# Kernel optimization log

Measured on AMD Instinct MI355X. Metric: run time of the kernel, lower is better.

The kernel has to match this reference:

```python
import jax, jax.numpy as jnp
import numpy as np

# static config (levels=4, CDA=False branch -> self_attn_4, scale=4, f=False)
SHAPES = [(80, 80), (40, 40), (20, 20), (10, 10)]
D = 256; NH = 8; NL = 4; NP = 4; DFF = 1024; DH = D // NH
L = sum(h * w for h, w in SHAPES)  # 8500
B = 1


def layer_norm(x, g, b, eps=1e-5):
    m = jnp.mean(x, axis=-1, keepdims=True)
    v = jnp.mean((x - m) ** 2, axis=-1, keepdims=True)
    return (x - m) * jax.lax.rsqrt(v + eps) * g + b


def ms_deform_attn_core(value, loc, attn):
    # value: [B, L, NH, DH]; loc: [B, Lq, NH, NL, NP, 2] in [0,1]; attn: [B, Lq, NH, NL, NP]
    Bq, Lq = loc.shape[0], loc.shape[1]
    out = jnp.zeros((Bq, NH, Lq, DH), value.dtype)
    start = 0
    for lvl, (Hl, Wl) in enumerate(SHAPES):
        v = value[:, start:start + Hl * Wl]          # [B, HW, NH, DH]
        start += Hl * Wl
        v = v.transpose(0, 2, 1, 3)                  # [B, NH, HW, DH]
        ll = loc[:, :, :, lvl]                       # [B, Lq, NH, NP, 2]
        # grid_sample semantics: align_corners=False, padding_mode='zeros'
        x = ll[..., 0] * Wl - 0.5
        y = ll[..., 1] * Hl - 0.5
        x0 = jnp.floor(x); y0 = jnp.floor(y)
        acc = jnp.zeros((Bq, NH, Lq, NP, DH), value.dtype)
        for dy in (0, 1):
            for dx in (0, 1):
                xi = x0 + dx; yi = y0 + dy
                w = (1.0 - jnp.abs(x - xi)) * (1.0 - jnp.abs(y - yi))  # [B,Lq,NH,NP]
                valid = (xi >= 0) & (xi < Wl) & (yi >= 0) & (yi < Hl)
                xi_c = jnp.clip(xi, 0, Wl - 1).astype(jnp.int32)
                yi_c = jnp.clip(yi, 0, Hl - 1).astype(jnp.int32)
                lin = (yi_c * Wl + xi_c).transpose(0, 2, 1, 3).reshape(Bq, NH, Lq * NP)
                g = jnp.take_along_axis(v, lin[..., None], axis=2).reshape(Bq, NH, Lq, NP, DH)
                wv = (w * valid.astype(w.dtype)).transpose(0, 2, 1, 3)[..., None]
                acc = acc + g * wv
        aw = attn[:, :, :, lvl].transpose(0, 2, 1, 3)[..., None]  # [B,NH,Lq,NP,1]
        out = out + jnp.sum(acc * aw, axis=3)
    return out.transpose(0, 2, 1, 3).reshape(Bq, Lq, NH * DH)


def setup_inputs():
    key = jax.random.key(0)
    ks = jax.random.split(key, 24)
    s = 0.02
    d = {}
    d['src'] = jax.random.normal(ks[0], (B, L, D), jnp.float32)
    d['pos'] = jax.random.normal(ks[1], (B, L, D), jnp.float32)
    d['reference_points'] = jax.random.uniform(ks[2], (B, L, NL, 2), jnp.float32)
    d['spatial_shapes'] = jnp.array(SHAPES, jnp.int32)
    d['level_start_index'] = jnp.array(np.cumsum([0] + [h * w for h, w in SHAPES[:-1]]), jnp.int32)
    d['scale'] = 4
    # MSDeformAttn params
    d['Wo'] = jax.random.normal(ks[3], (D, NH * NL * NP * 2), jnp.float32) * s
    d['bo'] = jax.random.normal(ks[4], (NH * NL * NP * 2,), jnp.float32) * s
    d['Wa'] = jax.random.normal(ks[5], (D, NH * NL * NP), jnp.float32) * s
    d['ba'] = jax.random.normal(ks[6], (NH * NL * NP,), jnp.float32) * s
    d['Wv'] = jax.random.normal(ks[7], (D, D), jnp.float32) * s
    d['bv'] = jnp.zeros((D,), jnp.float32)
    d['Wout'] = jax.random.normal(ks[8], (D, D), jnp.float32) * s
    d['bout'] = jnp.zeros((D,), jnp.float32)
    # FFN + LayerNorms
    d['W1'] = jax.random.normal(ks[9], (D, DFF), jnp.float32) * s
    d['b1'] = jnp.zeros((DFF,), jnp.float32)
    d['W2'] = jax.random.normal(ks[10], (DFF, D), jnp.float32) * s
    d['b2'] = jnp.zeros((D,), jnp.float32)
    d['g1'] = jnp.ones((D,), jnp.float32); d['be1'] = jnp.zeros((D,), jnp.float32)
    d['g2'] = jnp.ones((D,), jnp.float32); d['be2'] = jnp.zeros((D,), jnp.float32)
    return d


def reference(src, pos, reference_points, spatial_shapes, level_start_index, scale,
              Wo, bo, Wa, ba, Wv, bv, Wout, bout, W1, b1, W2, b2, g1, be1, g2, be2):
    Bq, Lq, _ = src.shape
    q = src + pos  # with_pos_embed
    # sampling offsets & attention weights (softmax over levels*points)
    off = (q @ Wo + bo).reshape(Bq, Lq, NH, NL, NP, 2)
    attn = jax.nn.softmax((q @ Wa + ba).reshape(Bq, Lq, NH, NL * NP), axis=-1)
    attn = attn.reshape(Bq, Lq, NH, NL, NP)
    value = (src @ Wv + bv).reshape(Bq, L, NH, DH)
    # offset normalizer is (W, H) per level
    normalizer = jnp.stack([spatial_shapes[:, 1], spatial_shapes[:, 0]], -1).astype(src.dtype)
    loc = reference_points[:, :, None, :, None, :] + off / normalizer[None, None, None, :, None, :]
    src2 = ms_deform_attn_core(value, loc, attn) @ Wout + bout
    # residual + norm1 (dropout = eval identity)
    x = layer_norm(src + src2, g1, be1)
    # FFN
    ffn = jax.nn.relu(x @ W1 + b1) @ W2 + b2
    x = layer_norm(x + ffn, g2, be2)
    return x
```

## Files before the change

kernel.cpp:

```cpp
#include <hip/hip_runtime.h>
#include <hip/hip_bf16.h>
#include <string.h>

#define D 256
#define NH 8
#define DH 32
#define NL 4
#define NP 4
#define DFF 1024
#define LTOT 8500

typedef __bf16 bf16x8 __attribute__((ext_vector_type(8)));
typedef float floatx4 __attribute__((ext_vector_type(4)));

__device__ inline unsigned bpack(float a, float b) {
    __hip_bfloat16 ha = __float2bfloat16(a), hb = __float2bfloat16(b);
    unsigned short ua, ub;
    memcpy(&ua, &ha, 2); memcpy(&ub, &hb, 2);
    return (unsigned)ua | ((unsigned)ub << 16);
}

__global__ void prep(const float* __restrict__ src, const float* __restrict__ pos,
                     unsigned* __restrict__ qb, unsigned* __restrict__ srcb, int n4) {
    int i = blockIdx.x * blockDim.x + threadIdx.x;
    if (i >= n4) return;
    float4 s = *(const float4*)(src + i * 4);
    float4 p = *(const float4*)(pos + i * 4);
    uint2 sb, qb2;
    sb.x = bpack(s.x, s.y); sb.y = bpack(s.z, s.w);
    qb2.x = bpack(s.x + p.x, s.y + p.y); qb2.y = bpack(s.z + p.z, s.w + p.w);
    *(uint2*)(srcb + i * 2) = sb;
    *(uint2*)(qb + i * 2) = qb2;
}

__global__ void transpose_all(const float* W0, const float* W1_, const float* W2_,
                              const float* W3, const float* W4, const float* W5,
                              __hip_bfloat16* T0, __hip_bfloat16* T1, __hip_bfloat16* T2,
                              __hip_bfloat16* T3, __hip_bfloat16* T4, __hip_bfloat16* T5) {
    const int cum[7] = {0, 64, 96, 160, 224, 480, 736};
    int id = blockIdx.x;
    int mi = 0;
    while (id >= cum[mi + 1]) mi++;
    int lid = id - cum[mi];
    const float* W; __hip_bfloat16* T; int K, N;
    switch (mi) {
        case 0: W = W0; T = T0; K = 256;  N = 256;  break;
        case 1: W = W1_; T = T1; K = 256; N = 128;  break;
        case 2: W = W2_; T = T2; K = 256; N = 256;  break;
        case 3: W = W3; T = T3; K = 256;  N = 256;  break;
        case 4: W = W4; T = T4; K = 256;  N = 1024; break;
        default: W = W5; T = T5; K = 1024; N = 256; break;
    }
    int ntx = N >> 5;
    int n0 = (lid % ntx) * 32, k0 = (lid / ntx) * 32;
    __shared__ float t[32][33];
    int tx = threadIdx.x & 31, ty = threadIdx.x >> 5;
#pragma unroll
    for (int i = 0; i < 32; i += 8)
        t[ty + i][tx] = W[(size_t)(k0 + ty + i) * N + n0 + tx];
    __syncthreads();
#pragma unroll
    for (int i = 0; i < 32; i += 8)
        T[(size_t)(n0 + ty + i) * K + k0 + tx] = __float2bfloat16(t[tx][ty + i]);
}

template<int BM, int BN>
__global__ __launch_bounds__(256) void gemm_mfma(
    const __hip_bfloat16* __restrict__ A, const __hip_bfloat16* __restrict__ BT,
    const float* __restrict__ bias, float* __restrict__ Cf, __hip_bfloat16* __restrict__ Cb,
    int M, int N, int K, int relu) {
    constexpr int BK = 32;
    constexpr int LDA = BK + 8;
    __shared__ __hip_bfloat16 sA[BM * LDA];
    __shared__ __hip_bfloat16 sB[BN * LDA];

    int tid = threadIdx.x;
    int wave = tid >> 6, lane = tid & 63;
    int m0 = blockIdx.y * BM;
    int n0 = blockIdx.x * BN;
    constexpr int WM = BM / 2, WN = BN / 2;
    int wm = (wave >> 1) * WM;
    int wn = (wave & 1) * WN;
    constexpr int TM = WM / 16, TN = WN / 16;

    floatx4 acc[TM][TN];
#pragma unroll
    for (int i = 0; i < TM; i++)
#pragma unroll
        for (int j = 0; j < TN; j++)
#pragma unroll
            for (int e = 0; e < 4; e++) acc[i][j][e] = 0.f;

    constexpr int RA = BM / 64, RB = BN / 64;
    int rowT = tid >> 2;
    int c16 = tid & 3;
    int lrow = lane & 15;
    int lk = (lane >> 4) * 8;

    for (int k0 = 0; k0 < K; k0 += BK) {
#pragma unroll
        for (int r = 0; r < RA; r++) {
            int row = r * 64 + rowT;
            int grow = m0 + row; if (grow >= M) grow = M - 1;
            bf16x8 v = *(const bf16x8*)(A + (size_t)grow * K + k0 + c16 * 8);
            *(bf16x8*)(&sA[row * LDA + c16 * 8]) = v;
        }
#pragma unroll
        for (int r = 0; r < RB; r++) {
            int row = r * 64 + rowT;
            bf16x8 v = *(const bf16x8*)(BT + (size_t)(n0 + row) * K + k0 + c16 * 8);
            *(bf16x8*)(&sB[row * LDA + c16 * 8]) = v;
        }
        __syncthreads();

        bf16x8 af[TM], bfr[TN];
#pragma unroll
        for (int tm = 0; tm < TM; tm++)
            af[tm] = *(const bf16x8*)(&sA[(wm + tm * 16 + lrow) * LDA + lk]);
#pragma unroll
        for (int tn = 0; tn < TN; tn++)
            bfr[tn] = *(const bf16x8*)(&sB[(wn + tn * 16 + lrow) * LDA + lk]);
#pragma unroll
        for (int tm = 0; tm < TM; tm++)
#pragma unroll
            for (int tn = 0; tn < TN; tn++)
                acc[tm][tn] = __builtin_amdgcn_mfma_f32_16x16x32_bf16(af[tm], bfr[tn], acc[tm][tn], 0, 0, 0);
        __syncthreads();
    }

    int lcol = lane & 15;
    int lr4 = (lane >> 4) * 4;
#pragma unroll
    for (int tm = 0; tm < TM; tm++) {
#pragma unroll
        for (int i = 0; i < 4; i++) {
            int row = m0 + wm + tm * 16 + lr4 + i;
            if (row < M) {
#pragma unroll
                for (int tn = 0; tn < TN; tn++) {
                    int col = n0 + wn + tn * 16 + lcol;
                    float v = acc[tm][tn][i] + bias[col];
                    if (relu) v = fmaxf(v, 0.f);
                    if (Cf) Cf[(size_t)row * N + col] = v;
                    if (Cb) Cb[(size_t)row * N + col] = __float2bfloat16(v);
                }
            }
        }
    }
}

__global__ __launch_bounds__(256) void proj_fused(
    const __hip_bfloat16* __restrict__ qb, const __hip_bfloat16* __restrict__ srcb,
    const __hip_bfloat16* __restrict__ WoT, const __hip_bfloat16* __restrict__ WaT,
    const __hip_bfloat16* __restrict__ WvT,
    const float* __restrict__ bo, const float* __restrict__ ba, const float* __restrict__ bv,
    float* __restrict__ locb, float* __restrict__ attnb, __hip_bfloat16* __restrict__ valb,
    int M) {
    constexpr int BM = 64, BN = 64, BK = 32, K = 256;
    constexpr int LDA = BK + 8;
    __shared__ __hip_bfloat16 sA[BM * LDA];
    __shared__ __hip_bfloat16 sB[BN * LDA];

    int n0 = blockIdx.x * BN;
    int m0 = blockIdx.y * BM;

    const __hip_bfloat16* A;
    const __hip_bfloat16* BT;
    const float* bias;
    int ncol0, Nout;
    float* Cf; __hip_bfloat16* Cb;
    if (n0 < 256)      { A = qb;   BT = WoT; bias = bo; ncol0 = n0;       Nout = 256; Cf = locb;  Cb = nullptr; }
    else if (n0 < 384) { A = qb;   BT = WaT; bias = ba; ncol0 = n0 - 256; Nout = 128; Cf = attnb; Cb = nullptr; }
    else               { A = srcb; BT = WvT; bias = bv; ncol0 = n0 - 384; Nout = 256; Cf = nullptr; Cb = valb; }

    int tid = threadIdx.x;
    int wave = tid >> 6, lane = tid & 63;
    int wm = (wave >> 1) * 32;
    int wn = (wave & 1) * 32;

    floatx4 acc[2][2];
#pragma unroll
    for (int i = 0; i < 2; i++)
#pragma unroll
        for (int j = 0; j < 2; j++)
#pragma unroll
            for (int e = 0; e < 4; e++) acc[i][j][e] = 0.f;

    int rowT = tid >> 2, c16 = tid & 3;
    int lrow = lane & 15, lk = (lane >> 4) * 8;

    for (int k0 = 0; k0 < K; k0 += BK) {
        {
            int grow = m0 + rowT; if (grow >= M) grow = M - 1;
            *(bf16x8*)(&sA[rowT * LDA + c16 * 8]) =
                *(const bf16x8*)(A + (size_t)grow * K + k0 + c16 * 8);
            *(bf16x8*)(&sB[rowT * LDA + c16 * 8]) =
                *(const bf16x8*)(BT + (size_t)(ncol0 + rowT) * K + k0 + c16 * 8);
        }
        __syncthreads();
        bf16x8 af[2], bfr[2];
#pragma unroll
        for (int t = 0; t < 2; t++) {
            af[t]  = *(const bf16x8*)(&sA[(wm + t * 16 + lrow) * LDA + lk]);
            bfr[t] = *(const bf16x8*)(&sB[(wn + t * 16 + lrow) * LDA + lk]);
        }
#pragma unroll
        for (int tm = 0; tm < 2; tm++)
#pragma unroll
            for (int tn = 0; tn < 2; tn++)
                acc[tm][tn] = __builtin_amdgcn_mfma_f32_16x16x32_bf16(af[tm], bfr[tn], acc[tm][tn], 0, 0, 0);
        __syncthreads();
    }

    int lcol = lane & 15, lr4 = (lane >> 4) * 4;
#pragma unroll
    for (int tm = 0; tm < 2; tm++) {
#pragma unroll
        for (int i = 0; i < 4; i++) {
            int row = m0 + wm + tm * 16 + lr4 + i;
            if (row < M) {
#pragma unroll
                for (int tn = 0; tn < 2; tn++) {
                    int col = ncol0 + wn + tn * 16 + lcol;
                    float v = acc[tm][tn][i] + bias[col];
                    if (Cf) Cf[(size_t)row * Nout + col] = v;
                    else    Cb[(size_t)row * Nout + col] = __float2bfloat16(v);
                }
            }
        }
    }
}

__global__ __launch_bounds__(256) void deform(const __hip_bfloat16* __restrict__ value,
                                              const float* __restrict__ locraw,
                                              const float* __restrict__ logits,
                                              const float* __restrict__ refp,
                                              __hip_bfloat16* __restrict__ out) {
    __shared__ float wS[4][8][16][4];
    __shared__ int   aS[4][8][16][4];
    int tid = threadIdx.x;
    int q0 = blockIdx.x * 4;

    {
        int sub = tid >> 6, h = (tid >> 3) & 7, t8 = tid & 7;
        int q = q0 + sub;
        const float* lg = logits + q * 128 + h * 16;
        float l0 = lg[t8], l1 = lg[t8 + 8];
        float mx = fmaxf(l0, l1);
#pragma unroll
        for (int m = 1; m < 8; m <<= 1) mx = fmaxf(mx, __shfl_xor(mx, m, 64));
        float e0 = __expf(l0 - mx), e1 = __expf(l1 - mx);
        float s = e0 + e1;
#pragma unroll
        for (int m = 1; m < 8; m <<= 1) s += __shfl_xor(s, m, 64);
        float inv = 1.f / s;

        const int starts[4] = {0, 6400, 8000, 8400};
#pragma unroll
        for (int j = 0; j < 2; j++) {
            int pp = t8 + 8 * j;
            float a = (j ? e1 : e0) * inv;
            int l = pp >> 2;
            int Wl = 80 >> l;
            float nv = (float)Wl;
            float rx = refp[q * 8 + l * 2 + 0];
            float ry = refp[q * 8 + l * 2 + 1];
            float lx = rx + locraw[q * 256 + h * 32 + pp * 2 + 0] / nv;
            float ly = ry + locraw[q * 256 + h * 32 + pp * 2 + 1] / nv;
            float x = lx * nv - 0.5f;
            float y = ly * nv - 0.5f;
            float x0f = floorf(x), y0f = floorf(y);
            float fx = x - x0f, fy = y - y0f;
            int x0 = (int)x0f, y0 = (int)y0f;
            float wts[4] = {(1.f - fx) * (1.f - fy), fx * (1.f - fy),
                            (1.f - fx) * fy,         fx * fy};
            int st = starts[l];
#pragma unroll
            for (int t = 0; t < 4; t++) {
                int xi = x0 + (t & 1), yi = y0 + (t >> 1);
                bool valid = (xi >= 0) & (xi < Wl) & (yi >= 0) & (yi < Wl);
                int xc = min(max(xi, 0), Wl - 1), yc = min(max(yi, 0), Wl - 1);
                wS[sub][h][pp][t] = valid ? wts[t] * a : 0.f;
                aS[sub][h][pp][t] = (st + yc * Wl + xc) * 512 + h * 64;
            }
        }
    }
    __syncthreads();

    int sub = tid >> 6, h = (tid >> 3) & 7, l8 = tid & 7;
    int q = q0 + sub;
    const char* vb = (const char*)value;
    int lo = l8 * 8;
    float a0 = 0.f, a1 = 0.f, a2 = 0.f, a3 = 0.f;
#pragma unroll
    for (int p = 0; p < 16; p++) {
        floatx4 w = *(const floatx4*)&wS[sub][h][p][0];
        int4 av = *(const int4*)&aS[sub][h][p][0];
#pragma unroll
        for (int t = 0; t < 4; t++) {
            int ad = (t == 0) ? av.x : (t == 1) ? av.y : (t == 2) ? av.z : av.w;
            uint2 u = *(const uint2*)(vb + ad + lo);
            float wt = w[t];
            a0 += wt * __uint_as_float(u.x << 16);
            a1 += wt * __uint_as_float(u.x & 0xffff0000u);
            a2 += wt * __uint_as_float(u.y << 16);
            a3 += wt * __uint_as_float(u.y & 0xffff0000u);
        }
    }
    uint2 o;
    o.x = bpack(a0, a1);
    o.y = bpack(a2, a3);
    *(uint2*)((char*)out + q * 512 + h * 64 + l8 * 8) = o;
}

__global__ __launch_bounds__(256) void gemm_ln(
    const __hip_bfloat16* __restrict__ A, const __hip_bfloat16* __restrict__ BT,
    const float* __restrict__ bias, const float* __restrict__ resid,
    const float* __restrict__ g, const float* __restrict__ be,
    float* __restrict__ outf, __hip_bfloat16* __restrict__ outb,
    int M, int K) {
    constexpr int BM = 32, BK = 32, LDA = BK + 8;
    __shared__ __hip_bfloat16 sA[BM * LDA];
    __shared__ __hip_bfloat16 sB[256 * LDA];
    __shared__ float psum[4][32], psq[4][32], mS[32], rS[32];

    int tid = threadIdx.x;
    int wave = tid >> 6, lane = tid & 63;
    int m0 = blockIdx.x * BM;

    floatx4 acc[2][4];
#pragma unroll
    for (int i = 0; i < 2; i++)
#pragma unroll
        for (int j = 0; j < 4; j++)
#pragma unroll
            for (int e = 0; e < 4; e++) acc[i][j][e] = 0.f;

    int rowT = tid >> 2, c16 = tid & 3;
    int lrow = lane & 15, lk = (lane >> 4) * 8;

    for (int k0 = 0; k0 < K; k0 += BK) {
        if (tid < 128) {
            int grow = m0 + rowT; if (grow >= M) grow = M - 1;
            *(bf16x8*)(&sA[rowT * LDA + c16 * 8]) =
                *(const bf16x8*)(A + (size_t)grow * K + k0 + c16 * 8);
        }
#pragma unroll
        for (int r = 0; r < 4; r++) {
            int row = r * 64 + rowT;
            *(bf16x8*)(&sB[row * LDA + c16 * 8]) =
                *(const bf16x8*)(BT + (size_t)row * K + k0 + c16 * 8);
        }
        __syncthreads();
        bf16x8 af[2], bfr[4];
#pragma unroll
        for (int tm = 0; tm < 2; tm++)
            af[tm] = *(const bf16x8*)(&sA[(tm * 16 + lrow) * LDA + lk]);
#pragma unroll
        for (int tn = 0; tn < 4; tn++)
            bfr[tn] = *(const bf16x8*)(&sB[(wave * 64 + tn * 16 + lrow) * LDA + lk]);
#pragma unroll
        for (int tm = 0; tm < 2; tm++)
#pragma unroll
            for (int tn = 0; tn < 4; tn++)
                acc[tm][tn] = __builtin_amdgcn_mfma_f32_16x16x32_bf16(af[tm], bfr[tn], acc[tm][tn], 0, 0, 0);
        __syncthreads();
    }

    int lcol = lane & 15, quad = lane >> 4;
    float v[2][4][4];
#pragma unroll
    for (int tm = 0; tm < 2; tm++) {
#pragma unroll
        for (int i = 0; i < 4; i++) {
            int row = tm * 16 + quad * 4 + i;
            int grow = m0 + row; if (grow >= M) grow = M - 1;
#pragma unroll
            for (int tn = 0; tn < 4; tn++) {
                int col = wave * 64 + tn * 16 + lcol;
                v[tm][tn][i] = acc[tm][tn][i] + bias[col] + resid[(size_t)grow * 256 + col];
            }
        }
    }

#pragma unroll
    for (int tm = 0; tm < 2; tm++) {
#pragma unroll
        for (int i = 0; i < 4; i++) {
            float s = 0.f, s2 = 0.f;
#pragma unroll
            for (int tn = 0; tn < 4; tn++) { float x = v[tm][tn][i]; s += x; s2 += x * x; }
#pragma unroll
            for (int m = 1; m < 16; m <<= 1) {
                s  += __shfl_xor(s, m, 64);
                s2 += __shfl_xor(s2, m, 64);
            }
            if (lcol == 0) {
                int row = tm * 16 + quad * 4 + i;
                psum[wave][row] = s;
                psq[wave][row]  = s2;
            }
        }
    }
    __syncthreads();
    if (tid < 32) {
        float s  = psum[0][tid] + psum[1][tid] + psum[2][tid] + psum[3][tid];
        float s2 = psq[0][tid]  + psq[1][tid]  + psq[2][tid]  + psq[3][tid];
        float m = s * (1.f / 256.f);
        float var = fmaxf(s2 * (1.f / 256.f) - m * m, 0.f);
        mS[tid] = m;
        rS[tid] = rsqrtf(var + 1e-5f);
    }
    __syncthreads();

#pragma unroll
    for (int tm = 0; tm < 2; tm++) {
#pragma unroll
        for (int i = 0; i < 4; i++) {
            int row = tm * 16 + quad * 4 + i;
            int grow = m0 + row;
            if (grow < M) {
                float m = mS[row], r = rS[row];
#pragma unroll
                for (int tn = 0; tn < 4; tn++) {
                    int col = wave * 64 + tn * 16 + lcol;
                    float o = (v[tm][tn][i] - m) * r * g[col] + be[col];
                    outf[(size_t)grow * 256 + col] = o;
                    if (outb) outb[(size_t)grow * 256 + col] = __float2bfloat16(o);
                }
            }
        }
    }
}

extern "C" void kernel_launch(void* const* d_in, const int* in_sizes, int n_in,
                              void* d_out, int out_size, void* d_ws, size_t ws_size,
                              hipStream_t stream) {
    const float* src  = (const float*)d_in[0];
    const float* pos  = (const float*)d_in[1];
    const float* refp = (const float*)d_in[2];
    const float* Wo   = (const float*)d_in[6];
    const float* bo   = (const float*)d_in[7];
    const float* Wa   = (const float*)d_in[8];
    const float* ba   = (const float*)d_in[9];
    const float* Wv   = (const float*)d_in[10];
    const float* bv   = (const float*)d_in[11];
    const float* Wout = (const float*)d_in[12];
    const float* bout = (const float*)d_in[13];
    const float* W1   = (const float*)d_in[14];
    const float* b1   = (const float*)d_in[15];
    const float* W2   = (const float*)d_in[16];
    const float* b2   = (const float*)d_in[17];
    const float* g1   = (const float*)d_in[18];
    const float* be1  = (const float*)d_in[19];
    const float* g2   = (const float*)d_in[20];
    const float* be2  = (const float*)d_in[21];
    float* out = (float*)d_out;
    char* ws = (char*)d_ws;

    __hip_bfloat16* WoT   = (__hip_bfloat16*)(ws + 0);
    __hip_bfloat16* WaT   = (__hip_bfloat16*)(ws + 131072);
    __hip_bfloat16* WvT   = (__hip_bfloat16*)(ws + 196608);
    __hip_bfloat16* WoutT = (__hip_bfloat16*)(ws + 327680);
    __hip_bfloat16* W1T   = (__hip_bfloat16*)(ws + 458752);
    __hip_bfloat16* W2T   = (__hip_bfloat16*)(ws + 983040);
    __hip_bfloat16* qb    = (__hip_bfloat16*)(ws + 1507328);
    __hip_bfloat16* srcb  = (__hip_bfloat16*)(ws + 5859328);
    float*          locb  = (float*)(ws + 10211328);
    float*          attnb = (float*)(ws + 18915328);
    __hip_bfloat16* valb  = (__hip_bfloat16*)(ws + 23267328);
    __hip_bfloat16* hb    = (__hip_bfloat16*)(ws + 31971328);
    __hip_bfloat16* aob  = qb;
    float*          x1   = locb;
    __hip_bfloat16* x1b  = srcb;

    prep<<<2125, 256, 0, stream>>>(src, pos, (unsigned*)qb, (unsigned*)srcb, LTOT * D / 4);
    transpose_all<<<736, 256, 0, stream>>>(Wo, Wa, Wv, Wout, W1, W2,
                                           WoT, WaT, WvT, WoutT, W1T, W2T);

    proj_fused<<<dim3(10, 133), 256, 0, stream>>>(qb, srcb, WoT, WaT, WvT, bo, ba, bv,
                                                  locb, attnb, valb, LTOT);

    deform<<<2125, 256, 0, stream>>>(valb, locb, attnb, refp, aob);

    gemm_ln<<<266, 256, 0, stream>>>(aob, WoutT, bout, src, g1, be1, x1, x1b, LTOT, 256);
    gemm_mfma<128, 128><<<dim3(8, 67), 256, 0, stream>>>(x1b, W1T, b1, nullptr, hb, LTOT, 1024, 256, 1);
    gemm_ln<<<266, 256, 0, stream>>>(hb, W2T, b2, x1, g2, be2, out, nullptr, LTOT, 1024);
}
```

Before: 219.7 us.

## Fuse src+pos bf16 conversion into projection GEMM and widen LayerNorm GEMM to 8 waves

Removes the separate prep kernel. The projection GEMM now loads fp32 src (and pos for the offset and attention columns), adds and packs to bf16 while staging into shared memory, which avoids writing and re-reading the bf16 intermediates. The gemm_ln kernel goes from 256 to 512 threads with each wave owning 32 output columns instead of 64, giving more waves per 32-row block and fewer accumulators per thread. The trade-off is that the projection kernel re-reads fp32 inputs for every column tile (10 tiles), and the LayerNorm reduction now sums 8 partial results.

```diff
diff --git a/kernel.cpp b/kernel.cpp
--- a/kernel.cpp
+++ b/kernel.cpp
@@ -18,19 +18,6 @@
     unsigned short ua, ub;
     memcpy(&ua, &ha, 2); memcpy(&ub, &hb, 2);
     return (unsigned)ua | ((unsigned)ub << 16);
-}
-
-__global__ void prep(const float* __restrict__ src, const float* __restrict__ pos,
-                     unsigned* __restrict__ qb, unsigned* __restrict__ srcb, int n4) {
-    int i = blockIdx.x * blockDim.x + threadIdx.x;
-    if (i >= n4) return;
-    float4 s = *(const float4*)(src + i * 4);
-    float4 p = *(const float4*)(pos + i * 4);
-    uint2 sb, qb2;
-    sb.x = bpack(s.x, s.y); sb.y = bpack(s.z, s.w);
-    qb2.x = bpack(s.x + p.x, s.y + p.y); qb2.y = bpack(s.z + p.z, s.w + p.w);
-    *(uint2*)(srcb + i * 2) = sb;
-    *(uint2*)(qb + i * 2) = qb2;
 }
 
 __global__ void transpose_all(const float* W0, const float* W1_, const float* W2_,
@@ -71,8 +58,8 @@
     int M, int N, int K, int relu) {
     constexpr int BK = 32;
     constexpr int LDA = BK + 8;
-    __shared__ __hip_bfloat16 sA[BM * LDA];
-    __shared__ __hip_bfloat16 sB[BN * LDA];
+    __shared__ __align__(16) __hip_bfloat16 sA[BM * LDA];
+    __shared__ __align__(16) __hip_bfloat16 sB[BN * LDA];
 
     int tid = threadIdx.x;
     int wave = tid >> 6, lane = tid & 63;
@@ -150,7 +137,7 @@
 }
 
 __global__ __launch_bounds__(256) void proj_fused(
-    const __hip_bfloat16* __restrict__ qb, const __hip_bfloat16* __restrict__ srcb,
+    const float* __restrict__ src, const float* __restrict__ pos,
     const __hip_bfloat16* __restrict__ WoT, const __hip_bfloat16* __restrict__ WaT,
     const __hip_bfloat16* __restrict__ WvT,
     const float* __restrict__ bo, const float* __restrict__ ba, const float* __restrict__ bv,
@@ -158,20 +145,19 @@
     int M) {
     constexpr int BM = 64, BN = 64, BK = 32, K = 256;
     constexpr int LDA = BK + 8;
-    __shared__ __hip_bfloat16 sA[BM * LDA];
-    __shared__ __hip_bfloat16 sB[BN * LDA];
+    __shared__ __align__(16) __hip_bfloat16 sA[BM * LDA];
+    __shared__ __align__(16) __hip_bfloat16 sB[BN * LDA];
 
     int n0 = blockIdx.x * BN;
     int m0 = blockIdx.y * BM;
 
-    const __hip_bfloat16* A;
     const __hip_bfloat16* BT;
     const float* bias;
-    int ncol0, Nout;
+    int ncol0, Nout, usePos;
     float* Cf; __hip_bfloat16* Cb;
-    if (n0 < 256)      { A = qb;   BT = WoT; bias = bo; ncol0 = n0;       Nout = 256; Cf = locb;  Cb = nullptr; }
-    else if (n0 < 384) { A = qb;   BT = WaT; bias = ba; ncol0 = n0 - 256; Nout = 128; Cf = attnb; Cb = nullptr; }
-    else               { A = srcb; BT = WvT; bias = bv; ncol0 = n0 - 384; Nout = 256; Cf = nullptr; Cb = valb; }
+    if (n0 < 256)      { BT = WoT; bias = bo; ncol0 = n0;       Nout = 256; Cf = locb;  Cb = nullptr; usePos = 1; }
+    else if (n0 < 384) { BT = WaT; bias = ba; ncol0 = n0 - 256; Nout = 128; Cf = attnb; Cb = nullptr; usePos = 1; }
+    else               { BT = WvT; bias = bv; ncol0 = n0 - 384; Nout = 256; Cf = nullptr; Cb = valb; usePos = 0; }
 
     int tid = threadIdx.x;
     int wave = tid >> 6, lane = tid & 63;
@@ -192,8 +178,20 @@
     for (int k0 = 0; k0 < K; k0 += BK) {
         {
             int grow = m0 + rowT; if (grow >= M) grow = M - 1;
-            *(bf16x8*)(&sA[rowT * LDA + c16 * 8]) =
-                *(const bf16x8*)(A + (size_t)grow * K + k0 + c16 * 8);
+            const float* ap = src + (size_t)grow * K + k0 + c16 * 8;
+            float4 s0 = *(const float4*)ap;
+            float4 s1 = *(const float4*)(ap + 4);
+            if (usePos) {
+                const float* pp = pos + (size_t)grow * K + k0 + c16 * 8;
+                float4 p0 = *(const float4*)pp;
+                float4 p1 = *(const float4*)(pp + 4);
+                s0.x += p0.x; s0.y += p0.y; s0.z += p0.z; s0.w += p0.w;
+                s1.x += p1.x; s1.y += p1.y; s1.z += p1.z; s1.w += p1.w;
+            }
+            uint4 pk;
+            pk.x = bpack(s0.x, s0.y); pk.y = bpack(s0.z, s0.w);
+            pk.z = bpack(s1.x, s1.y); pk.w = bpack(s1.z, s1.w);
+            *(uint4*)(&sA[rowT * LDA + c16 * 8]) = pk;
             *(bf16x8*)(&sB[rowT * LDA + c16 * 8]) =
                 *(const bf16x8*)(BT + (size_t)(ncol0 + rowT) * K + k0 + c16 * 8);
         }
@@ -313,26 +311,26 @@
     *(uint2*)((char*)out + q * 512 + h * 64 + l8 * 8) = o;
 }
 
-__global__ __launch_bounds__(256) void gemm_ln(
+__global__ __launch_bounds__(512) void gemm_ln(
     const __hip_bfloat16* __restrict__ A, const __hip_bfloat16* __restrict__ BT,
     const float* __restrict__ bias, const float* __restrict__ resid,
     const float* __restrict__ g, const float* __restrict__ be,
     float* __restrict__ outf, __hip_bfloat16* __restrict__ outb,
     int M, int K) {
     constexpr int BM = 32, BK = 32, LDA = BK + 8;
-    __shared__ __hip_bfloat16 sA[BM * LDA];
-    __shared__ __hip_bfloat16 sB[256 * LDA];
-    __shared__ float psum[4][32], psq[4][32], mS[32], rS[32];
+    __shared__ __align__(16) __hip_bfloat16 sA[BM * LDA];
+    __shared__ __align__(16) __hip_bfloat16 sB[256 * LDA];
+    __shared__ float psum[8][32], psq[8][32], mS[32], rS[32];
 
     int tid = threadIdx.x;
     int wave = tid >> 6, lane = tid & 63;
     int m0 = blockIdx.x * BM;
 
-    floatx4 acc[2][4];
+    floatx4 acc[2][2];
 #pragma unroll
     for (int i = 0; i < 2; i++)
 #pragma unroll
-        for (int j = 0; j < 4; j++)
+        for (int j = 0; j < 2; j++)
 #pragma unroll
             for (int e = 0; e < 4; e++) acc[i][j][e] = 0.f;
 
@@ -346,29 +344,29 @@
                 *(const bf16x8*)(A + (size_t)grow * K + k0 + c16 * 8);
         }
 #pragma unroll
-        for (int r = 0; r < 4; r++) {
-            int row = r * 64 + rowT;
+        for (int r = 0; r < 2; r++) {
+            int row = r * 128 + rowT;
             *(bf16x8*)(&sB[row * LDA + c16 * 8]) =
                 *(const bf16x8*)(BT + (size_t)row * K + k0 + c16 * 8);
         }
         __syncthreads();
-        bf16x8 af[2], bfr[4];
+        bf16x8 af[2], bfr[2];
 #pragma unroll
         for (int tm = 0; tm < 2; tm++)
             af[tm] = *(const bf16x8*)(&sA[(tm * 16 + lrow) * LDA + lk]);
 #pragma unroll
-        for (int tn = 0; tn < 4; tn++)
-            bfr[tn] = *(const bf16x8*)(&sB[(wave * 64 + tn * 16 + lrow) * LDA + lk]);
+        for (int tn = 0; tn < 2; tn++)
+            bfr[tn] = *(const bf16x8*)(&sB[(wave * 32 + tn * 16 + lrow) * LDA + lk]);
 #pragma unroll
         for (int tm = 0; tm < 2; tm++)
 #pragma unroll
-            for (int tn = 0; tn < 4; tn++)
+            for (int tn = 0; tn < 2; tn++)
                 acc[tm][tn] = __builtin_amdgcn_mfma_f32_16x16x32_bf16(af[tm], bfr[tn], acc[tm][tn], 0, 0, 0);
         __syncthreads();
     }
 
     int lcol = lane & 15, quad = lane >> 4;
-    float v[2][4][4];
+    float v[2][2][4];
 #pragma unroll
     for (int tm = 0; tm < 2; tm++) {
 #pragma unroll
@@ -376,8 +374,8 @@
             int row = tm * 16 + quad * 4 + i;
             int grow = m0 + row; if (grow >= M) grow = M - 1;
 #pragma unroll
-            for (int tn = 0; tn < 4; tn++) {
-                int col = wave * 64 + tn * 16 + lcol;
+            for (int tn = 0; tn < 2; tn++) {
+                int col = wave * 32 + tn * 16 + lcol;
                 v[tm][tn][i] = acc[tm][tn][i] + bias[col] + resid[(size_t)grow * 256 + col];
             }
         }
@@ -389,7 +387,7 @@
         for (int i = 0; i < 4; i++) {
             float s = 0.f, s2 = 0.f;
 #pragma unroll
-            for (int tn = 0; tn < 4; tn++) { float x = v[tm][tn][i]; s += x; s2 += x * x; }
+            for (int tn = 0; tn < 2; tn++) { float x = v[tm][tn][i]; s += x; s2 += x * x; }
 #pragma unroll
             for (int m = 1; m < 16; m <<= 1) {
                 s  += __shfl_xor(s, m, 64);
@@ -404,8 +402,9 @@
     }
     __syncthreads();
     if (tid < 32) {
-        float s  = psum[0][tid] + psum[1][tid] + psum[2][tid] + psum[3][tid];
-        float s2 = psq[0][tid]  + psq[1][tid]  + psq[2][tid]  + psq[3][tid];
+        float s = 0.f, s2 = 0.f;
+#pragma unroll
+        for (int w = 0; w < 8; w++) { s += psum[w][tid]; s2 += psq[w][tid]; }
         float m = s * (1.f / 256.f);
         float var = fmaxf(s2 * (1.f / 256.f) - m * m, 0.f);
         mS[tid] = m;
@@ -422,8 +421,8 @@
             if (grow < M) {
                 float m = mS[row], r = rS[row];
 #pragma unroll
-                for (int tn = 0; tn < 4; tn++) {
-                    int col = wave * 64 + tn * 16 + lcol;
+                for (int tn = 0; tn < 2; tn++) {
+                    int col = wave * 32 + tn * 16 + lcol;
                     float o = (v[tm][tn][i] - m) * r * g[col] + be[col];
                     outf[(size_t)grow * 256 + col] = o;
                     if (outb) outb[(size_t)grow * 256 + col] = __float2bfloat16(o);
@@ -464,26 +463,23 @@
     __hip_bfloat16* WoutT = (__hip_bfloat16*)(ws + 327680);
     __hip_bfloat16* W1T   = (__hip_bfloat16*)(ws + 458752);
     __hip_bfloat16* W2T   = (__hip_bfloat16*)(ws + 983040);
-    __hip_bfloat16* qb    = (__hip_bfloat16*)(ws + 1507328);
-    __hip_bfloat16* srcb  = (__hip_bfloat16*)(ws + 5859328);
-    float*          locb  = (float*)(ws + 10211328);
-    float*          attnb = (float*)(ws + 18915328);
-    __hip_bfloat16* valb  = (__hip_bfloat16*)(ws + 23267328);
-    __hip_bfloat16* hb    = (__hip_bfloat16*)(ws + 31971328);
-    __hip_bfloat16* aob  = qb;
-    float*          x1   = locb;
-    __hip_bfloat16* x1b  = srcb;
-
-    prep<<<2125, 256, 0, stream>>>(src, pos, (unsigned*)qb, (unsigned*)srcb, LTOT * D / 4);
+    float*          locb  = (float*)(ws + 1507328);
+    float*          attnb = (float*)(ws + 10211328);
+    __hip_bfloat16* valb  = (__hip_bfloat16*)(ws + 14563328);
+    __hip_bfloat16* aob   = (__hip_bfloat16*)(ws + 18915328);
+    float*          x1    = (float*)(ws + 23267328);
+    __hip_bfloat16* x1b   = (__hip_bfloat16*)(ws + 31971328);
+    __hip_bfloat16* hb    = (__hip_bfloat16*)(ws + 36323328);
+
     transpose_all<<<736, 256, 0, stream>>>(Wo, Wa, Wv, Wout, W1, W2,
                                            WoT, WaT, WvT, WoutT, W1T, W2T);
 
-    proj_fused<<<dim3(10, 133), 256, 0, stream>>>(qb, srcb, WoT, WaT, WvT, bo, ba, bv,
+    proj_fused<<<dim3(10, 133), 256, 0, stream>>>(src, pos, WoT, WaT, WvT, bo, ba, bv,
                                                   locb, attnb, valb, LTOT);
 
     deform<<<2125, 256, 0, stream>>>(valb, locb, attnb, refp, aob);
 
-    gemm_ln<<<266, 256, 0, stream>>>(aob, WoutT, bout, src, g1, be1, x1, x1b, LTOT, 256);
+    gemm_ln<<<266, 512, 0, stream>>>(aob, WoutT, bout, src, g1, be1, x1, x1b, LTOT, 256);
     gemm_mfma<128, 128><<<dim3(8, 67), 256, 0, stream>>>(x1b, W1T, b1, nullptr, hb, LTOT, 1024, 256, 1);
-    gemm_ln<<<266, 256, 0, stream>>>(hb, W2T, b2, x1, g2, be2, out, nullptr, LTOT, 1024);
-}
+    gemm_ln<<<266, 512, 0, stream>>>(hb, W2T, b2, x1, g2, be2, out, nullptr, LTOT, 1024);
+}
```

Measured after the change: 219.1 us. No clear change (-0.3%).
